# Kernel tuning notes

Hardware: AMD Instinct MI355X
Metric: run time of the kernel (lower is better)

## Reference

```python
import jax, jax.numpy as jnp
import numpy as np

B, N, S, FIN, H, P = 16, 96, 4, 8, 32, 256  # graphs, nodes, edge feats, node feats, channels, pref pairs


def setup_inputs() -> dict:
    key = jax.random.key(0)
    ks = jax.random.split(key, 12)
    xf = jax.random.normal(ks[0], (B, N, FIN), jnp.float32)
    mask = (jax.random.uniform(ks[1], (B, N, 1)) < 0.9).astype(jnp.float32)
    x = jnp.concatenate([xf, mask], axis=-1)  # last column = node mask (GraphMasking)
    a = (jax.random.uniform(ks[2], (B, N, N)) < 0.1).astype(jnp.float32)  # dense binary adjacency
    e = jax.random.normal(ks[3], (B, N, N, S), jnp.float32)
    pref_a = jax.random.randint(ks[4], (P,), 0, B)
    pref_b = jax.random.randint(ks[5], (P,), 0, B)
    g = lambda k, sh: jax.random.normal(k, sh, jnp.float32) * 0.1
    return dict(
        x=x, a=a, e=e, pref_a=pref_a, pref_b=pref_b,
        W1=g(ks[6], (S, FIN * H)), b1=jnp.zeros((FIN * H,), jnp.float32),
        root1=g(ks[7], (FIN, H)), bias1=jnp.zeros((H,), jnp.float32),
        W2=g(ks[8], (S, H * H)), b2=jnp.zeros((H * H,), jnp.float32),
        root2=g(ks[9], (H, H)), bias2=jnp.zeros((H,), jnp.float32),
        Wd=g(ks[10], (H, 1)), bd=jnp.zeros((1,), jnp.float32),
    )


def ecc_conv(x, a, e, W, b, root, bias, mask, fin, fout):
    # Edge-conditioned filter: Dense(S -> fin*fout) per edge, reshaped [B,N,N,fout,fin]
    K = (e @ W + b).reshape(e.shape[0], e.shape[1], e.shape[2], fout, fin)
    # out[b,n,c] = sum_i a[b,n,i] * sum_f K[b,n,i,c,f] * x[b,i,f]
    out = jnp.einsum("bni,bnicf,bif->bnc", a, K, x)
    out = out + x @ root + bias   # root skip + bias
    out = out * mask              # keras mask propagated from GraphMasking
    return jax.nn.relu(out)


def reference(x, a, e, pref_a, pref_b, W1, b1, root1, bias1, W2, b2, root2, bias2, Wd, bd):
    mask = x[..., -1:]            # GraphMasking: strip mask column
    h = x[..., :-1]
    h = ecc_conv(h, a, e, W1, b1, root1, bias1, mask, FIN, H)
    h = ecc_conv(h, a, e, W2, b2, root2, bias2, mask, H, H)
    pooled = jnp.sum(h, axis=1)                 # GlobalSumPool -> [B, H]
    score = jax.nn.relu(pooled @ Wd + bd)       # Dense(1, relu) -> [B, 1]
    return score[pref_a] - score[pref_b]        # pref_lookup diff -> [P, 1]
```

## Files before the change

### kernel.cpp

```cpp
#include <hip/hip_runtime.h>

namespace {
constexpr int NB   = 16;
constexpr int NN   = 96;
constexpr int NS   = 4;
constexpr int NFIN = 8;
constexpr int NH   = 32;
constexpr int NP   = 256;
constexpr int NPB  = 8;
constexpr int NCH  = NN / NPB;
constexpr int NBLK = NB * NCH;


__global__ __launch_bounds__(256) void k1_layer1(
    const float* __restrict__ x, const float* __restrict__ a,
    const float* __restrict__ e,
    const float* __restrict__ W1, const float* __restrict__ b1,
    const float* __restrict__ root1, const float* __restrict__ bias1,
    float* __restrict__ h1g, unsigned* __restrict__ cnt)
{
  const int chunk = blockIdx.x, bb = blockIdx.y;
  const int t = threadIdx.x, g = t >> 5, lane = t & 31;
  const int gn = chunk * NPB + g;

  __shared__ __align__(16) float xraw[NN * 9];
  __shared__ __align__(16) float eL[NPB][NN * NS];
  __shared__ __align__(16) float TbA[NPB][NH];
  __shared__ __align__(16) float TbU[NPB][NFIN];

  if (chunk == 0 && bb == 0 && t == 0) *cnt = 0u;

  const float4* er4 = (const float4*)(e + (size_t)(bb * NN + gn) * NN * NS);
  float4 e0 = er4[lane], e1 = er4[lane + 32], e2 = er4[lane + 64];
  const float* ar = a + (size_t)(bb * NN + gn) * NN;
  float a0 = ar[lane], a1 = ar[lane + 32], a2 = ar[lane + 64];
  float4 xl;
  if (t < 216) xl = ((const float4*)(x + (size_t)bb * NN * 9))[t];

  const int c = lane;
  const float4* W1_4 = (const float4*)W1;
  const float4* b1_4 = (const float4*)b1;
  float4 w1r[8], b1r[2];
  float  r1r[NFIN];
  #pragma unroll
  for (int ss = 0; ss < 4; ++ss) {
    w1r[ss * 2 + 0] = W1_4[ss * 64 + c * 2 + 0];
    w1r[ss * 2 + 1] = W1_4[ss * 64 + c * 2 + 1];
  }
  b1r[0] = b1_4[c * 2 + 0];
  b1r[1] = b1_4[c * 2 + 1];
  #pragma unroll
  for (int ff = 0; ff < NFIN; ++ff) r1r[ff] = root1[ff * NH + c];
  const float biasv = bias1[c];

  float4* eL4 = (float4*)eL[g];
  eL4[lane] = e0; eL4[lane + 32] = e1; eL4[lane + 64] = e2;
  if (t < 216) ((float4*)xraw)[t] = xl;

  unsigned long long B0 = __ballot(a0 != 0.f);
  unsigned long long B1 = __ballot(a1 != 0.f);
  unsigned long long B2 = __ballot(a2 != 0.f);
  const bool hi = (t & 63) >= 32;
  unsigned m[3];
  m[0] = hi ? (unsigned)(B0 >> 32) : (unsigned)B0;
  m[1] = hi ? (unsigned)(B1 >> 32) : (unsigned)B1;
  m[2] = hi ? (unsigned)(B2 >> 32) : (unsigned)B2;

  __syncthreads();

  const int s = lane >> 3, f = lane & 7;
  float accT = 0.f, accU = 0.f;
  #pragma unroll
  for (int r = 0; r < 3; ++r) {
    unsigned mm = m[r];
    while (mm) {
      int idx = r * 32 + __builtin_ctz(mm);
      mm &= mm - 1;
      float xv = xraw[idx * 9 + f];
      float ev = eL[g][idx * 4 + s];
      accT = fmaf(ev, xv, accT);
      accU += xv;
    }
  }
  TbA[g][s * 8 + f] = accT;
  if (s == 0) TbU[g][f] = accU;

  float E = biasv;
  const float4* TA4 = (const float4*)TbA[g];
  #pragma unroll
  for (int k = 0; k < 8; ++k) {
    float4 w = w1r[k], tt = TA4[k];
    E = fmaf(w.x, tt.x, E); E = fmaf(w.y, tt.y, E);
    E = fmaf(w.z, tt.z, E); E = fmaf(w.w, tt.w, E);
  }
  const float4* TU4 = (const float4*)TbU[g];
  #pragma unroll
  for (int q = 0; q < 2; ++q) {
    float4 w = b1r[q], u = TU4[q];
    E = fmaf(w.x, u.x, E); E = fmaf(w.y, u.y, E);
    E = fmaf(w.z, u.z, E); E = fmaf(w.w, u.w, E);
  }
  #pragma unroll
  for (int ff = 0; ff < NFIN; ++ff) E = fmaf(xraw[gn * 9 + ff], r1r[ff], E);
  E *= xraw[gn * 9 + 8];
  h1g[((size_t)bb * NN + gn) * NH + c] = E > 0.f ? E : 0.f;
}

__global__ __launch_bounds__(256) void k2_layer2(
    const float* __restrict__ x, const float* __restrict__ a,
    const float* __restrict__ e,
    const float* __restrict__ W2, const float* __restrict__ b2,
    const float* __restrict__ root2, const float* __restrict__ bias2,
    const float* __restrict__ Wd, const float* __restrict__ bd,
    const int* __restrict__ pa, const int* __restrict__ pb,
    const float* __restrict__ h1g, float* __restrict__ poolp,
    unsigned* __restrict__ cnt, float* __restrict__ out)
{
  const int chunk = blockIdx.x, bb = blockIdx.y;
  const int t = threadIdx.x, g = t >> 5, lane = t & 31;
  const int gn = chunk * NPB + g;

  __shared__ __align__(16) float h1b[NN][NH];
  __shared__ __align__(16) float eL[NPB][NN * NS];
  __shared__ __align__(16) float4 T2s[NPB][32];
  __shared__ __align__(16) float4 U2s[NPB][8];
  __shared__ float h2s[NPB][NH];
  __shared__ float scoreS[NB];
  __shared__ int lastFlag;

  const float4* er4 = (const float4*)(e + (size_t)(bb * NN + gn) * NN * NS);
  float4 e0 = er4[lane], e1 = er4[lane + 32], e2 = er4[lane + 64];
  const float* ar = a + (size_t)(bb * NN + gn) * NN;
  float a0 = ar[lane], a1 = ar[lane + 32], a2 = ar[lane + 64];
  const float4* h14 = (const float4*)(h1g + (size_t)bb * NN * NH);
  float4 h0 = h14[t], h1_ = h14[t + 256], h2_ = h14[t + 512];
  const float xm = x[((size_t)bb * NN + gn) * 9 + 8];

  const int c = lane;
  const float4* b2_4 = (const float4*)b2;
  float4 b2r[8];
  float  r2r[NH];
  #pragma unroll
  for (int q = 0; q < 8; ++q) b2r[q] = b2_4[c * 8 + q];
  #pragma unroll
  for (int ff = 0; ff < NH; ++ff) r2r[ff] = root2[ff * NH + c];
  const float biasv = bias2[c];

  float4* eL4 = (float4*)eL[g];
  eL4[lane] = e0; eL4[lane + 32] = e1; eL4[lane + 64] = e2;
  float4* h1b4 = (float4*)h1b;
  h1b4[t] = h0; h1b4[t + 256] = h1_; h1b4[t + 512] = h2_;

  unsigned long long B0 = __ballot(a0 != 0.f);
  unsigned long long B1 = __ballot(a1 != 0.f);
  unsigned long long B2 = __ballot(a2 != 0.f);
  const bool hi = (t & 63) >= 32;
  unsigned m[3];
  m[0] = hi ? (unsigned)(B0 >> 32) : (unsigned)B0;
  m[1] = hi ? (unsigned)(B1 >> 32) : (unsigned)B1;
  m[2] = hi ? (unsigned)(B2 >> 32) : (unsigned)B2;

  __syncthreads();

  const int s = lane >> 3, f4 = lane & 7;
  float4 accT = make_float4(0.f, 0.f, 0.f, 0.f);
  float4 accU = make_float4(0.f, 0.f, 0.f, 0.f);
  #pragma unroll
  for (int r = 0; r < 3; ++r) {
    unsigned mm = m[r];
    while (mm) {
      int idx = r * 32 + __builtin_ctz(mm);
      mm &= mm - 1;
      float4 h4 = *(const float4*)&h1b[idx][f4 * 4];
      float ev = eL[g][idx * 4 + s];
      accT.x = fmaf(ev, h4.x, accT.x); accT.y = fmaf(ev, h4.y, accT.y);
      accT.z = fmaf(ev, h4.z, accT.z); accT.w = fmaf(ev, h4.w, accT.w);
      accU.x += h4.x; accU.y += h4.y; accU.z += h4.z; accU.w += h4.w;
    }
  }
  T2s[g][s * 8 + f4] = accT;
  if (s == 0) U2s[g][f4] = accU;

  float E = biasv;
  const float4* W2_4 = (const float4*)W2;
  #pragma unroll
  for (int ss = 0; ss < 4; ++ss)
    #pragma unroll
    for (int q = 0; q < 8; ++q) {
      float4 w  = W2_4[ss * 256 + c * 8 + q];
      float4 tt = T2s[g][ss * 8 + q];
      E = fmaf(w.x, tt.x, E); E = fmaf(w.y, tt.y, E);
      E = fmaf(w.z, tt.z, E); E = fmaf(w.w, tt.w, E);
    }
  #pragma unroll
  for (int q = 0; q < 8; ++q) {
    float4 w = b2r[q], u = U2s[g][q];
    E = fmaf(w.x, u.x, E); E = fmaf(w.y, u.y, E);
    E = fmaf(w.z, u.z, E); E = fmaf(w.w, u.w, E);
  }
  #pragma unroll
  for (int ff = 0; ff < NH; ++ff) E = fmaf(h1b[gn][ff], r2r[ff], E);
  E *= xm;
  h2s[g][c] = E > 0.f ? E : 0.f;
  __syncthreads();

  if (t < NH) {
    float p = 0.f;
    #pragma unroll
    for (int n = 0; n < NPB; ++n) p += h2s[n][t];
    poolp[(size_t)(bb * NCH + chunk) * NH + t] = p;
  }
  __syncthreads();

  if (t == 0) {
    __threadfence();
    unsigned old = atomicAdd(cnt, 1u);
    lastFlag = (old == (unsigned)(NBLK - 1));
  }
  __syncthreads();
  if (!lastFlag) return;
  __threadfence();

  #pragma unroll
  for (int half = 0; half < 2; ++half) {
    const int sb = (t >> 5) + half * 8;
    float v = 0.f;
    #pragma unroll
    for (int k = 0; k < NCH; ++k) v += poolp[(sb * NCH + k) * NH + lane];
    v *= Wd[lane];
    v += __shfl_xor(v, 16);
    v += __shfl_xor(v, 8);
    v += __shfl_xor(v, 4);
    v += __shfl_xor(v, 2);
    v += __shfl_xor(v, 1);
    if (lane == 0) {
      float sc = v + bd[0];
      scoreS[sb] = sc > 0.f ? sc : 0.f;
    }
  }
  __syncthreads();
  out[t] = scoreS[pa[t]] - scoreS[pb[t]];
}

}

extern "C" void kernel_launch(void* const* d_in, const int* in_sizes, int n_in,
                              void* d_out, int out_size, void* d_ws, size_t ws_size,
                              hipStream_t stream) {
  (void)in_sizes; (void)n_in; (void)out_size; (void)ws_size;
  const float* x     = (const float*)d_in[0];
  const float* a     = (const float*)d_in[1];
  const float* e     = (const float*)d_in[2];
  const int*   pa    = (const int*)d_in[3];
  const int*   pb    = (const int*)d_in[4];
  const float* W1    = (const float*)d_in[5];
  const float* b1    = (const float*)d_in[6];
  const float* root1 = (const float*)d_in[7];
  const float* bias1 = (const float*)d_in[8];
  const float* W2    = (const float*)d_in[9];
  const float* b2    = (const float*)d_in[10];
  const float* root2 = (const float*)d_in[11];
  const float* bias2 = (const float*)d_in[12];
  const float* Wd    = (const float*)d_in[13];
  const float* bd    = (const float*)d_in[14];

  float*    h1g   = (float*)d_ws;
  float*    poolp = h1g + NB * NN * NH;
  unsigned* cnt   = (unsigned*)(poolp + NB * NCH * NH + 32);
  float*    out   = (float*)d_out;

  dim3 grid(NCH, NB);
  k1_layer1<<<grid, 256, 0, stream>>>(x, a, e, W1, b1, root1, bias1, h1g, cnt);
  k2_layer2<<<grid, 256, 0, stream>>>(x, a, e, W2, b2, root2, bias2, Wd, bd,
                                      pa, pb, h1g, poolp, cnt, out);
}
```

Baseline: 23.35 us.

## Fuse both ECC layers into one kernel with per-graph spin barrier

Merges the layer-1 and layer-2 kernels into a single launch. Each graph's 12 blocks meet at a per-graph atomic counter barrier before reading the layer-1 output through device-scope atomic loads. The e tile, adjacency masks and x tile stay in shared memory and registers, so layer 2 no longer reloads them. A small init kernel now resets the counters. The barrier relies on all 192 blocks being co-resident and adds spin-wait and atomic overhead, but it removes one kernel boundary and the redundant global loads.

```diff
diff --git a/kernel.cpp b/kernel.cpp
--- a/kernel.cpp
+++ b/kernel.cpp
@@ -10,25 +10,51 @@
 constexpr int NPB  = 8;
 constexpr int NCH  = NN / NPB;
 constexpr int NBLK = NB * NCH;
-
-
-__global__ __launch_bounds__(256) void k1_layer1(
+constexpr int CNT_STRIDE = 16;
+
+
+__device__ __forceinline__ void st_wt(float* p, float v) {
+  __hip_atomic_store((unsigned int*)p, __float_as_uint(v),
+                     __ATOMIC_RELAXED, __HIP_MEMORY_SCOPE_AGENT);
+}
+__device__ __forceinline__ float ld_wt(const float* p) {
+  return __uint_as_float(__hip_atomic_load((unsigned int*)p,
+                     __ATOMIC_RELAXED, __HIP_MEMORY_SCOPE_AGENT));
+}
+
+__global__ void k_init(unsigned* __restrict__ cnts) {
+  const int t = threadIdx.x;
+  for (int j = t; j < NB * CNT_STRIDE + CNT_STRIDE; j += 64) cnts[j] = 0u;
+}
+
+__global__ __launch_bounds__(256) void k_main(
     const float* __restrict__ x, const float* __restrict__ a,
     const float* __restrict__ e,
     const float* __restrict__ W1, const float* __restrict__ b1,
     const float* __restrict__ root1, const float* __restrict__ bias1,
-    float* __restrict__ h1g, unsigned* __restrict__ cnt)
+    const float* __restrict__ W2, const float* __restrict__ b2,
+    const float* __restrict__ root2, const float* __restrict__ bias2,
+    const float* __restrict__ Wd, const float* __restrict__ bd,
+    const int* __restrict__ pa, const int* __restrict__ pb,
+    float* __restrict__ h1g, float* __restrict__ poolp,
+    unsigned* __restrict__ cnt1, unsigned* __restrict__ cnt2,
+    float* __restrict__ out)
 {
   const int chunk = blockIdx.x, bb = blockIdx.y;
   const int t = threadIdx.x, g = t >> 5, lane = t & 31;
   const int gn = chunk * NPB + g;
+  const int c  = lane;
 
   __shared__ __align__(16) float xraw[NN * 9];
   __shared__ __align__(16) float eL[NPB][NN * NS];
+  __shared__ __align__(16) float h1b[NN * NH];
   __shared__ __align__(16) float TbA[NPB][NH];
   __shared__ __align__(16) float TbU[NPB][NFIN];
-
-  if (chunk == 0 && bb == 0 && t == 0) *cnt = 0u;
+  __shared__ __align__(16) float4 T2s[NPB][32];
+  __shared__ __align__(16) float4 U2s[NPB][8];
+  __shared__ float h2s[NPB][NH];
+  __shared__ float scoreS[NB];
+  __shared__ int lastFlag;
 
   const float4* er4 = (const float4*)(e + (size_t)(bb * NN + gn) * NN * NS);
   float4 e0 = er4[lane], e1 = er4[lane + 32], e2 = er4[lane + 64];
@@ -37,7 +63,6 @@
   float4 xl;
   if (t < 216) xl = ((const float4*)(x + (size_t)bb * NN * 9))[t];
 
-  const int c = lane;
   const float4* W1_4 = (const float4*)W1;
   const float4* b1_4 = (const float4*)b1;
   float4 w1r[8], b1r[2];
@@ -51,7 +76,7 @@
   b1r[1] = b1_4[c * 2 + 1];
   #pragma unroll
   for (int ff = 0; ff < NFIN; ++ff) r1r[ff] = root1[ff * NH + c];
-  const float biasv = bias1[c];
+  const float bias1v = bias1[c];
 
   float4* eL4 = (float4*)eL[g];
   eL4[lane] = e0; eL4[lane + 32] = e1; eL4[lane + 64] = e2;
@@ -68,75 +93,56 @@
 
   __syncthreads();
 
-  const int s = lane >> 3, f = lane & 7;
-  float accT = 0.f, accU = 0.f;
-  #pragma unroll
-  for (int r = 0; r < 3; ++r) {
-    unsigned mm = m[r];
-    while (mm) {
-      int idx = r * 32 + __builtin_ctz(mm);
-      mm &= mm - 1;
-      float xv = xraw[idx * 9 + f];
-      float ev = eL[g][idx * 4 + s];
-      accT = fmaf(ev, xv, accT);
-      accU += xv;
-    }
-  }
-  TbA[g][s * 8 + f] = accT;
-  if (s == 0) TbU[g][f] = accU;
-
-  float E = biasv;
-  const float4* TA4 = (const float4*)TbA[g];
-  #pragma unroll
-  for (int k = 0; k < 8; ++k) {
-    float4 w = w1r[k], tt = TA4[k];
-    E = fmaf(w.x, tt.x, E); E = fmaf(w.y, tt.y, E);
-    E = fmaf(w.z, tt.z, E); E = fmaf(w.w, tt.w, E);
-  }
-  const float4* TU4 = (const float4*)TbU[g];
-  #pragma unroll
-  for (int q = 0; q < 2; ++q) {
-    float4 w = b1r[q], u = TU4[q];
-    E = fmaf(w.x, u.x, E); E = fmaf(w.y, u.y, E);
-    E = fmaf(w.z, u.z, E); E = fmaf(w.w, u.w, E);
-  }
-  #pragma unroll
-  for (int ff = 0; ff < NFIN; ++ff) E = fmaf(xraw[gn * 9 + ff], r1r[ff], E);
-  E *= xraw[gn * 9 + 8];
-  h1g[((size_t)bb * NN + gn) * NH + c] = E > 0.f ? E : 0.f;
-}
-
-__global__ __launch_bounds__(256) void k2_layer2(
-    const float* __restrict__ x, const float* __restrict__ a,
-    const float* __restrict__ e,
-    const float* __restrict__ W2, const float* __restrict__ b2,
-    const float* __restrict__ root2, const float* __restrict__ bias2,
-    const float* __restrict__ Wd, const float* __restrict__ bd,
-    const int* __restrict__ pa, const int* __restrict__ pb,
-    const float* __restrict__ h1g, float* __restrict__ poolp,
-    unsigned* __restrict__ cnt, float* __restrict__ out)
-{
-  const int chunk = blockIdx.x, bb = blockIdx.y;
-  const int t = threadIdx.x, g = t >> 5, lane = t & 31;
-  const int gn = chunk * NPB + g;
-
-  __shared__ __align__(16) float h1b[NN][NH];
-  __shared__ __align__(16) float eL[NPB][NN * NS];
-  __shared__ __align__(16) float4 T2s[NPB][32];
-  __shared__ __align__(16) float4 U2s[NPB][8];
-  __shared__ float h2s[NPB][NH];
-  __shared__ float scoreS[NB];
-  __shared__ int lastFlag;
-
-  const float4* er4 = (const float4*)(e + (size_t)(bb * NN + gn) * NN * NS);
-  float4 e0 = er4[lane], e1 = er4[lane + 32], e2 = er4[lane + 64];
-  const float* ar = a + (size_t)(bb * NN + gn) * NN;
-  float a0 = ar[lane], a1 = ar[lane + 32], a2 = ar[lane + 64];
-  const float4* h14 = (const float4*)(h1g + (size_t)bb * NN * NH);
-  float4 h0 = h14[t], h1_ = h14[t + 256], h2_ = h14[t + 512];
-  const float xm = x[((size_t)bb * NN + gn) * 9 + 8];
-
-  const int c = lane;
+  {
+    const int s = lane >> 3, f = lane & 7;
+    float accT = 0.f, accU = 0.f;
+    #pragma unroll
+    for (int r = 0; r < 3; ++r) {
+      unsigned mm = m[r];
+      while (mm) {
+        int idx = r * 32 + __builtin_ctz(mm);
+        mm &= mm - 1;
+        float xv = xraw[idx * 9 + f];
+        float ev = eL[g][idx * 4 + s];
+        accT = fmaf(ev, xv, accT);
+        accU += xv;
+      }
+    }
+    TbA[g][s * 8 + f] = accT;
+    if (s == 0) TbU[g][f] = accU;
+
+    float E = bias1v;
+    const float4* TA4 = (const float4*)TbA[g];
+    #pragma unroll
+    for (int k = 0; k < 8; ++k) {
+      float4 w = w1r[k], tt = TA4[k];
+      E = fmaf(w.x, tt.x, E); E = fmaf(w.y, tt.y, E);
+      E = fmaf(w.z, tt.z, E); E = fmaf(w.w, tt.w, E);
+    }
+    const float4* TU4 = (const float4*)TbU[g];
+    #pragma unroll
+    for (int q = 0; q < 2; ++q) {
+      float4 w = b1r[q], u = TU4[q];
+      E = fmaf(w.x, u.x, E); E = fmaf(w.y, u.y, E);
+      E = fmaf(w.z, u.z, E); E = fmaf(w.w, u.w, E);
+    }
+    #pragma unroll
+    for (int ff = 0; ff < NFIN; ++ff) E = fmaf(xraw[gn * 9 + ff], r1r[ff], E);
+    E *= xraw[gn * 9 + 8];
+    st_wt(&h1g[((size_t)bb * NN + gn) * NH + c], E > 0.f ? E : 0.f);
+  }
+
+  asm volatile("s_waitcnt vmcnt(0)" ::: "memory");
+  __syncthreads();
+  if (t == 0) {
+    unsigned* c1 = cnt1 + bb * CNT_STRIDE;
+    __hip_atomic_fetch_add(c1, 1u, __ATOMIC_RELAXED, __HIP_MEMORY_SCOPE_AGENT);
+    while (__hip_atomic_load(c1, __ATOMIC_RELAXED,
+                             __HIP_MEMORY_SCOPE_AGENT) < (unsigned)NCH)
+      __builtin_amdgcn_s_sleep(2);
+  }
+  __syncthreads();
+
   const float4* b2_4 = (const float4*)b2;
   float4 b2r[8];
   float  r2r[NH];
@@ -144,89 +150,82 @@
   for (int q = 0; q < 8; ++q) b2r[q] = b2_4[c * 8 + q];
   #pragma unroll
   for (int ff = 0; ff < NH; ++ff) r2r[ff] = root2[ff * NH + c];
-  const float biasv = bias2[c];
-
-  float4* eL4 = (float4*)eL[g];
-  eL4[lane] = e0; eL4[lane + 32] = e1; eL4[lane + 64] = e2;
-  float4* h1b4 = (float4*)h1b;
-  h1b4[t] = h0; h1b4[t + 256] = h1_; h1b4[t + 512] = h2_;
-
-  unsigned long long B0 = __ballot(a0 != 0.f);
-  unsigned long long B1 = __ballot(a1 != 0.f);
-  unsigned long long B2 = __ballot(a2 != 0.f);
-  const bool hi = (t & 63) >= 32;
-  unsigned m[3];
-  m[0] = hi ? (unsigned)(B0 >> 32) : (unsigned)B0;
-  m[1] = hi ? (unsigned)(B1 >> 32) : (unsigned)B1;
-  m[2] = hi ? (unsigned)(B2 >> 32) : (unsigned)B2;
-
-  __syncthreads();
-
-  const int s = lane >> 3, f4 = lane & 7;
-  float4 accT = make_float4(0.f, 0.f, 0.f, 0.f);
-  float4 accU = make_float4(0.f, 0.f, 0.f, 0.f);
-  #pragma unroll
-  for (int r = 0; r < 3; ++r) {
-    unsigned mm = m[r];
-    while (mm) {
-      int idx = r * 32 + __builtin_ctz(mm);
-      mm &= mm - 1;
-      float4 h4 = *(const float4*)&h1b[idx][f4 * 4];
-      float ev = eL[g][idx * 4 + s];
-      accT.x = fmaf(ev, h4.x, accT.x); accT.y = fmaf(ev, h4.y, accT.y);
-      accT.z = fmaf(ev, h4.z, accT.z); accT.w = fmaf(ev, h4.w, accT.w);
-      accU.x += h4.x; accU.y += h4.y; accU.z += h4.z; accU.w += h4.w;
-    }
-  }
-  T2s[g][s * 8 + f4] = accT;
-  if (s == 0) U2s[g][f4] = accU;
-
-  float E = biasv;
-  const float4* W2_4 = (const float4*)W2;
-  #pragma unroll
-  for (int ss = 0; ss < 4; ++ss)
+  const float bias2v = bias2[c];
+
+  {
+    const float* h1base = h1g + (size_t)bb * NN * NH;
+    #pragma unroll
+    for (int r = 0; r < 12; ++r) h1b[r * 256 + t] = ld_wt(h1base + r * 256 + t);
+  }
+  __syncthreads();
+
+  {
+    const int s = lane >> 3, f4 = lane & 7;
+    float4 accT = make_float4(0.f, 0.f, 0.f, 0.f);
+    float4 accU = make_float4(0.f, 0.f, 0.f, 0.f);
+    #pragma unroll
+    for (int r = 0; r < 3; ++r) {
+      unsigned mm = m[r];
+      while (mm) {
+        int idx = r * 32 + __builtin_ctz(mm);
+        mm &= mm - 1;
+        float4 h4 = *(const float4*)&h1b[idx * NH + f4 * 4];
+        float ev = eL[g][idx * 4 + s];
+        accT.x = fmaf(ev, h4.x, accT.x); accT.y = fmaf(ev, h4.y, accT.y);
+        accT.z = fmaf(ev, h4.z, accT.z); accT.w = fmaf(ev, h4.w, accT.w);
+        accU.x += h4.x; accU.y += h4.y; accU.z += h4.z; accU.w += h4.w;
+      }
+    }
+    T2s[g][s * 8 + f4] = accT;
+    if (s == 0) U2s[g][f4] = accU;
+
+    float E = bias2v;
+    const float4* W2_4 = (const float4*)W2;
+    #pragma unroll
+    for (int ss = 0; ss < 4; ++ss)
+      #pragma unroll
+      for (int q = 0; q < 8; ++q) {
+        float4 w  = W2_4[ss * 256 + c * 8 + q];
+        float4 tt = T2s[g][ss * 8 + q];
+        E = fmaf(w.x, tt.x, E); E = fmaf(w.y, tt.y, E);
+        E = fmaf(w.z, tt.z, E); E = fmaf(w.w, tt.w, E);
+      }
     #pragma unroll
     for (int q = 0; q < 8; ++q) {
-      float4 w  = W2_4[ss * 256 + c * 8 + q];
-      float4 tt = T2s[g][ss * 8 + q];
-      E = fmaf(w.x, tt.x, E); E = fmaf(w.y, tt.y, E);
-      E = fmaf(w.z, tt.z, E); E = fmaf(w.w, tt.w, E);
-    }
-  #pragma unroll
-  for (int q = 0; q < 8; ++q) {
-    float4 w = b2r[q], u = U2s[g][q];
-    E = fmaf(w.x, u.x, E); E = fmaf(w.y, u.y, E);
-    E = fmaf(w.z, u.z, E); E = fmaf(w.w, u.w, E);
-  }
-  #pragma unroll
-  for (int ff = 0; ff < NH; ++ff) E = fmaf(h1b[gn][ff], r2r[ff], E);
-  E *= xm;
-  h2s[g][c] = E > 0.f ? E : 0.f;
+      float4 w = b2r[q], u = U2s[g][q];
+      E = fmaf(w.x, u.x, E); E = fmaf(w.y, u.y, E);
+      E = fmaf(w.z, u.z, E); E = fmaf(w.w, u.w, E);
+    }
+    #pragma unroll
+    for (int ff = 0; ff < NH; ++ff) E = fmaf(h1b[gn * NH + ff], r2r[ff], E);
+    E *= xraw[gn * 9 + 8];
+    h2s[g][c] = E > 0.f ? E : 0.f;
+  }
   __syncthreads();
 
   if (t < NH) {
     float p = 0.f;
     #pragma unroll
     for (int n = 0; n < NPB; ++n) p += h2s[n][t];
-    poolp[(size_t)(bb * NCH + chunk) * NH + t] = p;
-  }
+    st_wt(&poolp[(size_t)(bb * NCH + chunk) * NH + t], p);
+  }
+  asm volatile("s_waitcnt vmcnt(0)" ::: "memory");
   __syncthreads();
 
   if (t == 0) {
-    __threadfence();
-    unsigned old = atomicAdd(cnt, 1u);
+    unsigned old = __hip_atomic_fetch_add(cnt2, 1u, __ATOMIC_RELAXED,
+                                          __HIP_MEMORY_SCOPE_AGENT);
     lastFlag = (old == (unsigned)(NBLK - 1));
   }
   __syncthreads();
   if (!lastFlag) return;
-  __threadfence();
 
   #pragma unroll
   for (int half = 0; half < 2; ++half) {
     const int sb = (t >> 5) + half * 8;
     float v = 0.f;
     #pragma unroll
-    for (int k = 0; k < NCH; ++k) v += poolp[(sb * NCH + k) * NH + lane];
+    for (int k = 0; k < NCH; ++k) v += ld_wt(&poolp[(sb * NCH + k) * NH + lane]);
     v *= Wd[lane];
     v += __shfl_xor(v, 16);
     v += __shfl_xor(v, 8);
@@ -266,11 +265,13 @@
 
   float*    h1g   = (float*)d_ws;
   float*    poolp = h1g + NB * NN * NH;
-  unsigned* cnt   = (unsigned*)(poolp + NB * NCH * NH + 32);
+  unsigned* cnts  = (unsigned*)(poolp + NB * NCH * NH);
+  unsigned* cnt1  = cnts;
+  unsigned* cnt2  = cnts + NB * CNT_STRIDE;
   float*    out   = (float*)d_out;
 
-  dim3 grid(NCH, NB);
-  k1_layer1<<<grid, 256, 0, stream>>>(x, a, e, W1, b1, root1, bias1, h1g, cnt);
-  k2_layer2<<<grid, 256, 0, stream>>>(x, a, e, W2, b2, root2, bias2, Wd, bd,
-                                      pa, pb, h1g, poolp, cnt, out);
-}
+  k_init<<<1, 64, 0, stream>>>(cnts);
+  k_main<<<dim3(NCH, NB), 256, 0, stream>>>(
+      x, a, e, W1, b1, root1, bias1, W2, b2, root2, bias2, Wd, bd,
+      pa, pb, h1g, poolp, cnt1, cnt2, out);
+}
```

New measurement: 26.13 us. +11.9%, slower.
